# Kernel optimization log

Measured on AMD Instinct MI355X. Metric: run time of the kernel, lower is better.

Reference implementation:

```python
import jax, jax.numpy as jnp
import numpy as np

N_NODES = 100000
N_EDGES = 1600000
N_GRAPHS = 256


def gcn_conv(x, src, dst, edge_weight, W, b, num_nodes):
    """PyG GCNConv: add self-loops, symmetric degree normalization,
    linear transform, scatter-add aggregation, bias."""
    loop = jnp.arange(num_nodes)
    s = jnp.concatenate([src, loop])
    d = jnp.concatenate([dst, loop])
    ew = jnp.concatenate([edge_weight, jnp.ones((num_nodes,), dtype=edge_weight.dtype)])
    deg = jax.ops.segment_sum(ew, d, num_segments=num_nodes)  # [N]
    dinv = jnp.where(deg > 0, deg ** -0.5, 0.0)
    norm = dinv[s] * ew * dinv[d]  # [E+N]
    h = x @ W  # [N, out]
    msg = h[s] * norm[:, None]  # gather + scale
    out = jax.ops.segment_sum(msg, d, num_segments=num_nodes)  # scatter-add
    return out + b


def global_mean_pool(x, batch, num_graphs):
    s = jax.ops.segment_sum(x, batch, num_segments=num_graphs)
    cnt = jax.ops.segment_sum(jnp.ones((x.shape[0],), dtype=x.dtype), batch, num_segments=num_graphs)
    return s / jnp.maximum(cnt, 1.0)[:, None]


def setup_inputs() -> dict:
    key = jax.random.key(0)
    ks = jax.random.split(key, 12)
    x = jax.random.normal(ks[0], (N_NODES, 128), dtype=jnp.float32)
    edge_index = jax.random.randint(ks[1], (2, N_EDGES), 0, N_NODES, dtype=jnp.int64)
    edge_attr = jax.random.uniform(ks[2], (N_EDGES,), dtype=jnp.float32)
    batch = jnp.sort(jax.random.randint(ks[3], (N_NODES,), 0, N_GRAPHS, dtype=jnp.int64))
    def lin(k, fan_in, fan_out):
        lim = 1.0 / np.sqrt(fan_in)
        kw, kb = jax.random.split(k)
        W = jax.random.uniform(kw, (fan_in, fan_out), minval=-lim, maxval=lim, dtype=jnp.float32)
        b = jax.random.uniform(kb, (fan_out,), minval=-lim, maxval=lim, dtype=jnp.float32)
        return W, b
    W1, b1 = lin(ks[4], 128, 64)
    W2, b2 = lin(ks[5], 64, 64)
    W3, b3 = lin(ks[6], 64, 64)
    Wl, bl = lin(ks[7], 64, 10)
    return {"x": x, "edge_index": edge_index, "edge_attr": edge_attr, "batch": batch,
            "W1": W1, "b1": b1, "W2": W2, "b2": b2, "W3": W3, "b3": b3, "Wl": Wl, "bl": bl}


def reference(x, edge_index, edge_attr, batch, W1, b1, W2, b2, W3, b3, Wl, bl):
    src, dst = edge_index[0], edge_index[1]
    n = x.shape[0]
    h = jax.nn.relu(gcn_conv(x, src, dst, edge_attr, W1, b1, n))
    h = jax.nn.relu(gcn_conv(h, src, dst, edge_attr, W2, b2, n))
    h = jax.nn.relu(gcn_conv(h, src, dst, edge_attr, W3, b3, n))
    g = global_mean_pool(h, batch, N_GRAPHS)  # [G, 64]
    return g @ Wl + bl  # [G, num_classes]
```

## Files before the change

### kernel.cpp

```cpp
#include <hip/hip_runtime.h>
#include <hip/hip_bf16.h>

#define N_NODES  100000
#define N_EDGES  1600000
#define N_GRAPHS 256
#define F 64
#define NBUCK  782
#define CHUNK  4096
#define NCHUNK 391
#define GB     391


__global__ __launch_bounds__(1024) void k_hist(const int* __restrict__ dst, int* __restrict__ hist) {
    __shared__ int lh[NBUCK];
    int tid = threadIdx.x, chunk = blockIdx.x;
    for (int j = tid; j < NBUCK; j += 1024) lh[j] = 0;
    __syncthreads();
    int e0 = chunk * CHUNK;
#pragma unroll
    for (int i = 0; i < CHUNK / 1024; i++) {
        int e = e0 + i * 1024 + tid;
        if (e < N_EDGES) atomicAdd(&lh[dst[e] >> 7], 1);
    }
    __syncthreads();
    for (int j = tid; j < NBUCK; j += 1024) hist[chunk * NBUCK + j] = lh[j];
}

__global__ __launch_bounds__(512) void k_colscan(int* __restrict__ hist, int* __restrict__ btot) {
    __shared__ int ts[512];
    int b = blockIdx.x, tid = threadIdx.x;
    int v = (tid < NCHUNK) ? hist[tid * NBUCK + b] : 0;
    ts[tid] = v;
    __syncthreads();
    int x = v;
    for (int off = 1; off < 512; off <<= 1) {
        int t = (tid >= off) ? ts[tid - off] : 0;
        __syncthreads();
        x += t; ts[tid] = x;
        __syncthreads();
    }
    if (tid < NCHUNK) hist[tid * NBUCK + b] = x - v;
    if (tid == 511) btot[b] = x;
}

__global__ __launch_bounds__(512) void k_bscan_gstart(const int* __restrict__ btot, int* __restrict__ base,
                                                      const int* __restrict__ batch, int* __restrict__ gstart) {
    if (blockIdx.x == 1) {
        int g = threadIdx.x;
        if (g > N_GRAPHS) return;
        int lo = 0, hi = N_NODES;
        while (lo < hi) {
            int mid = (lo + hi) >> 1;
            if (batch[mid] < g) lo = mid + 1; else hi = mid;
        }
        gstart[g] = lo;
        return;
    }
    __shared__ int ts[256];
    int tid = threadIdx.x;
    int v[4], loc[4], run = 0;
    if (tid < 256) {
#pragma unroll
        for (int k = 0; k < 4; k++) {
            int c = tid * 4 + k;
            v[k] = (c < NBUCK) ? btot[c] : 0;
            loc[k] = run; run += v[k];
        }
        ts[tid] = run;
    }
    __syncthreads();
    int x = run;
    for (int off = 1; off < 256; off <<= 1) {
        int t = (tid >= off && tid < 256) ? ts[tid - off] : 0;
        __syncthreads();
        if (tid < 256) { x += t; ts[tid] = x; }
        __syncthreads();
    }
    if (tid < 256) {
        int texcl = x - run;
#pragma unroll
        for (int k = 0; k < 4; k++) {
            int c = tid * 4 + k;
            if (c < NBUCK) base[c] = texcl + loc[k];
        }
        if (tid == 255) base[NBUCK] = x;
    }
}

__global__ __launch_bounds__(1024) void k_partition(const int* __restrict__ src, const int* __restrict__ dst,
                                                    const float* __restrict__ ew,
                                                    const int* __restrict__ hist, const int* __restrict__ base,
                                                    long long* __restrict__ part) {
    __shared__ int cursor[NBUCK];
    int tid = threadIdx.x, chunk = blockIdx.x;
    for (int j = tid; j < NBUCK; j += 1024) cursor[j] = base[j] + hist[chunk * NBUCK + j];
    __syncthreads();
    int e0 = chunk * CHUNK;
#pragma unroll
    for (int i = 0; i < CHUNK / 1024; i++) {
        int e = e0 + i * 1024 + tid;
        if (e < N_EDGES) {
            int d = dst[e];
            int pos = atomicAdd(&cursor[d >> 7], 1);
            unsigned lo = (unsigned)src[e] | ((unsigned)(d & 127) << 17);
            long long rec = (long long)((unsigned long long)lo |
                            ((unsigned long long)__float_as_uint(ew[e]) << 32));
            part[pos] = rec;
        }
    }
}

__global__ __launch_bounds__(512) void k_deg(const long long* __restrict__ part,
                                             const int* __restrict__ base,
                                             float* __restrict__ dinv_g, int* __restrict__ row_off) {
    __shared__ float fdeg[128];
    __shared__ int   cnt[128];
    __shared__ int   sc[128];
    int b = blockIdx.x, tid = threadIdx.x;
    if (tid < 128) { fdeg[tid] = 1.0f; cnt[tid] = 0; }
    __syncthreads();
    int e0 = base[b], e1 = base[b + 1];
    for (int k = e0 + tid; k < e1; k += 512) {
        long long rec = part[k];
        int d7 = ((int)rec >> 17) & 127;
        atomicAdd(&fdeg[d7], __uint_as_float((unsigned)(rec >> 32)));
        atomicAdd(&cnt[d7], 1);
    }
    __syncthreads();
    int myc = 0, x = 0;
    if (tid < 128) {
        int node = b * 128 + tid;
        if (node < N_NODES) dinv_g[node] = rsqrtf(fdeg[tid]);
        myc = cnt[tid]; x = myc; sc[tid] = x;
    }
    __syncthreads();
    for (int off = 1; off < 128; off <<= 1) {
        int t = (tid < 128 && tid >= off) ? sc[tid - off] : 0;
        __syncthreads();
        if (tid < 128) { x += t; sc[tid] = x; }
        __syncthreads();
    }
    if (tid < 128) {
        int node = b * 128 + tid;
        if (node < N_NODES) row_off[node] = e0 + (x - myc);
    }
    if (b == 0 && tid == 0) row_off[N_NODES] = N_EDGES;
}

__global__ __launch_bounds__(512) void k_scat(const long long* __restrict__ part,
                                              const int* __restrict__ base,
                                              const float* __restrict__ dinv_g,
                                              const int* __restrict__ row_off,
                                              int2* __restrict__ esec) {
    __shared__ int cursor[128];
    int b = blockIdx.x, tid = threadIdx.x;
    if (tid < 128) {
        int node = b * 128 + tid;
        cursor[tid] = row_off[node < N_NODES ? node : N_NODES];
    }
    __syncthreads();
    int e0 = base[b], e1 = base[b + 1];
    for (int k = e0 + tid; k < e1; k += 512) {
        long long rec = part[k];
        int lo = (int)rec;
        int d7 = (lo >> 17) & 127;
        int s  = lo & 0x1FFFF;
        float w = __uint_as_float((unsigned)(rec >> 32));
        float coef = w * dinv_g[s];
        int pos = atomicAdd(&cursor[d7], 1);
        esec[pos] = make_int2(s << 7, __float_as_int(coef));
    }
    if (b == 0 && tid < 32) esec[N_EDGES + tid] = make_int2(0, 0);
}

__global__ __launch_bounds__(256) void k_gemm1(const float* __restrict__ X,
                                               const float* __restrict__ W,
                                               __hip_bfloat16* __restrict__ H) {
    constexpr int K = 128;
    constexpr int KC = 32;
    constexpr int XP = KC + 4;
    __shared__ float Xs[256 * XP];
    __shared__ float Ws[KC * F];
    const int tid  = threadIdx.x;
    const int fgrp = tid & 7;
    const int ngrp = tid >> 3;
    const int f0   = fgrp * 8;
    const int nb   = blockIdx.x * 256;

    float acc[8][8];
#pragma unroll
    for (int i = 0; i < 8; i++)
#pragma unroll
        for (int j = 0; j < 8; j++) acc[i][j] = 0.0f;

    for (int kc = 0; kc < K; kc += KC) {
        if (kc) __syncthreads();
#pragma unroll
        for (int pass = 0; pass < 8; pass++) {
            int idx = tid + pass * 256;
            int r = idx >> 3, q = idx & 7;
            int gr = nb + r; if (gr >= N_NODES) gr = N_NODES - 1;
            float4 v = *(const float4*)&X[(size_t)gr * K + kc + q * 4];
            *(float4*)&Xs[r * XP + q * 4] = v;
        }
#pragma unroll
        for (int pass = 0; pass < 2; pass++) {
            int idx = tid + pass * 256;
            float4 v = *(const float4*)&W[(size_t)(kc + (idx >> 4)) * F + (idx & 15) * 4];
            *(float4*)&Ws[idx * 4] = v;
        }
        __syncthreads();
#pragma unroll
        for (int k = 0; k < KC; k += 4) {
            float4 wa[4], wb[4];
#pragma unroll
            for (int kk = 0; kk < 4; kk++) {
                wa[kk] = *(const float4*)&Ws[(k + kk) * F + f0];
                wb[kk] = *(const float4*)&Ws[(k + kk) * F + f0 + 4];
            }
#pragma unroll
            for (int i = 0; i < 8; i++) {
                float4 xv = *(const float4*)&Xs[(ngrp + 32 * i) * XP + k];
#pragma unroll
                for (int kk = 0; kk < 4; kk++) {
                    float xk = (kk == 0) ? xv.x : (kk == 1) ? xv.y : (kk == 2) ? xv.z : xv.w;
                    acc[i][0] = fmaf(xk, wa[kk].x, acc[i][0]);
                    acc[i][1] = fmaf(xk, wa[kk].y, acc[i][1]);
                    acc[i][2] = fmaf(xk, wa[kk].z, acc[i][2]);
                    acc[i][3] = fmaf(xk, wa[kk].w, acc[i][3]);
                    acc[i][4] = fmaf(xk, wb[kk].x, acc[i][4]);
                    acc[i][5] = fmaf(xk, wb[kk].y, acc[i][5]);
                    acc[i][6] = fmaf(xk, wb[kk].z, acc[i][6]);
                    acc[i][7] = fmaf(xk, wb[kk].w, acc[i][7]);
                }
            }
        }
    }
#pragma unroll
    for (int i = 0; i < 8; i++) {
        int gn = nb + ngrp + 32 * i;
        if (gn < N_NODES) {
            __hip_bfloat16 hb[8];
#pragma unroll
            for (int j = 0; j < 8; j++) hb[j] = __float2bfloat16(acc[i][j]);
            *(uint4*)&H[(size_t)gn * F + f0] = *(uint4*)hb;
        }
    }
}

template <int K>
__global__ __launch_bounds__(256) void k_gemm(const unsigned short* __restrict__ X,
                                              const float* __restrict__ W,
                                              __hip_bfloat16* __restrict__ H) {
    constexpr int KC = 32;
    constexpr int XP = KC + 4;
    __shared__ float Xs[256 * XP];
    __shared__ float Ws[KC * F];
    const int tid  = threadIdx.x;
    const int fgrp = tid & 7;
    const int ngrp = tid >> 3;
    const int f0   = fgrp * 8;
    const int nb   = blockIdx.x * 256;

    float acc[8][8];
#pragma unroll
    for (int i = 0; i < 8; i++)
#pragma unroll
        for (int j = 0; j < 8; j++) acc[i][j] = 0.0f;

    for (int kc = 0; kc < K; kc += KC) {
        if (kc) __syncthreads();
#pragma unroll
        for (int pass = 0; pass < 4; pass++) {
            int idx = tid + pass * 256;
            int r = idx >> 2, q = idx & 3;
            int gr = nb + r; if (gr >= N_NODES) gr = N_NODES - 1;
            uint4 v = *(const uint4*)&X[(size_t)gr * K + kc + q * 8];
            float* dp = &Xs[r * XP + q * 8];
            dp[0] = __uint_as_float(v.x << 16);
            dp[1] = __uint_as_float(v.x & 0xffff0000u);
            dp[2] = __uint_as_float(v.y << 16);
            dp[3] = __uint_as_float(v.y & 0xffff0000u);
            dp[4] = __uint_as_float(v.z << 16);
            dp[5] = __uint_as_float(v.z & 0xffff0000u);
            dp[6] = __uint_as_float(v.w << 16);
            dp[7] = __uint_as_float(v.w & 0xffff0000u);
        }
#pragma unroll
        for (int pass = 0; pass < 2; pass++) {
            int idx = tid + pass * 256;
            float4 v = *(const float4*)&W[(size_t)(kc + (idx >> 4)) * F + (idx & 15) * 4];
            *(float4*)&Ws[idx * 4] = v;
        }
        __syncthreads();
#pragma unroll
        for (int k = 0; k < KC; k += 4) {
            float4 wa[4], wb[4];
#pragma unroll
            for (int kk = 0; kk < 4; kk++) {
                wa[kk] = *(const float4*)&Ws[(k + kk) * F + f0];
                wb[kk] = *(const float4*)&Ws[(k + kk) * F + f0 + 4];
            }
#pragma unroll
            for (int i = 0; i < 8; i++) {
                float4 xv = *(const float4*)&Xs[(ngrp + 32 * i) * XP + k];
#pragma unroll
                for (int kk = 0; kk < 4; kk++) {
                    float xk = (kk == 0) ? xv.x : (kk == 1) ? xv.y : (kk == 2) ? xv.z : xv.w;
                    acc[i][0] = fmaf(xk, wa[kk].x, acc[i][0]);
                    acc[i][1] = fmaf(xk, wa[kk].y, acc[i][1]);
                    acc[i][2] = fmaf(xk, wa[kk].z, acc[i][2]);
                    acc[i][3] = fmaf(xk, wa[kk].w, acc[i][3]);
                    acc[i][4] = fmaf(xk, wb[kk].x, acc[i][4]);
                    acc[i][5] = fmaf(xk, wb[kk].y, acc[i][5]);
                    acc[i][6] = fmaf(xk, wb[kk].z, acc[i][6]);
                    acc[i][7] = fmaf(xk, wb[kk].w, acc[i][7]);
                }
            }
        }
    }
#pragma unroll
    for (int i = 0; i < 8; i++) {
        int gn = nb + ngrp + 32 * i;
        if (gn < N_NODES) {
            __hip_bfloat16 hb[8];
#pragma unroll
            for (int j = 0; j < 8; j++) hb[j] = __float2bfloat16(acc[i][j]);
            *(uint4*)&H[(size_t)gn * F + f0] = *(uint4*)hb;
        }
    }
}

__global__ __launch_bounds__(256) void k_agg(const __hip_bfloat16* __restrict__ H,
                                             const int* __restrict__ row_off,
                                             const int2* __restrict__ esec,
                                             const float* __restrict__ dinv,
                                             const float* __restrict__ bias,
                                             __hip_bfloat16* __restrict__ O) {
    int wv   = threadIdx.x >> 6;
    int lane = threadIdx.x & 63;
    int np   = blockIdx.x * 16 + wv * 4;
    int q  = lane >> 3;
    int f8 = lane & 7;
    int r0 = __builtin_amdgcn_readfirstlane(row_off[np]);
    int r1 = __builtin_amdgcn_readfirstlane(row_off[np + 1]);
    int r2 = __builtin_amdgcn_readfirstlane(row_off[np + 2]);
    int r3 = __builtin_amdgcn_readfirstlane(row_off[np + 3]);
    int r4 = __builtin_amdgcn_readfirstlane(row_off[np + 4]);
    const char* Hbase = (const char*)H;

    float a0[8], a1[8], a2[8], a3[8];
#pragma unroll
    for (int u = 0; u < 8; u++) { a0[u] = 0.0f; a1[u] = 0.0f; a2[u] = 0.0f; a3[u] = 0.0f; }

    int l0 = r1 - r0, l1 = r2 - r1, l2 = r3 - r2, l3 = r4 - r3;
    int ml = l0 > l1 ? l0 : l1;
    if (l2 > ml) ml = l2;
    if (l3 > ml) ml = l3;
    int iters = (ml + 7) >> 3;
    int j0 = r0 + q, j1 = r1 + q, j2 = r2 + q, j3 = r3 + q;

    int2 ev0 = esec[j0 < N_EDGES ? j0 : N_EDGES];
    int2 ev1 = esec[j1 < N_EDGES ? j1 : N_EDGES];
    int2 ev2 = esec[j2 < N_EDGES ? j2 : N_EDGES];
    int2 ev3 = esec[j3 < N_EDGES ? j3 : N_EDGES];

    for (int it = 0; it < iters; it++) {
        int n0 = j0 + 8, n1 = j1 + 8, n2 = j2 + 8, n3 = j3 + 8;
        int2 en0 = esec[n0 < N_EDGES ? n0 : N_EDGES];
        int2 en1 = esec[n1 < N_EDGES ? n1 : N_EDGES];
        int2 en2 = esec[n2 < N_EDGES ? n2 : N_EDGES];
        int2 en3 = esec[n3 < N_EDGES ? n3 : N_EDGES];

        bool t0 = j0 < r1, t1 = j1 < r2, t2 = j2 < r3, t3 = j3 < r4;
        float c0 = t0 ? __int_as_float(ev0.y) : 0.0f;
        float c1 = t1 ? __int_as_float(ev1.y) : 0.0f;
        float c2 = t2 ? __int_as_float(ev2.y) : 0.0f;
        float c3 = t3 ? __int_as_float(ev3.y) : 0.0f;
        unsigned o0 = t0 ? (unsigned)ev0.x : 0u;
        unsigned o1 = t1 ? (unsigned)ev1.x : 0u;
        unsigned o2 = t2 ? (unsigned)ev2.x : 0u;
        unsigned o3 = t3 ? (unsigned)ev3.x : 0u;
        uint4 h0 = *(const uint4*)(Hbase + o0 + (f8 << 4));
        uint4 h1 = *(const uint4*)(Hbase + o1 + (f8 << 4));
        uint4 h2 = *(const uint4*)(Hbase + o2 + (f8 << 4));
        uint4 h3 = *(const uint4*)(Hbase + o3 + (f8 << 4));
        a0[0] = fmaf(c0, __uint_as_float(h0.x << 16),         a0[0]);
        a0[1] = fmaf(c0, __uint_as_float(h0.x & 0xffff0000u), a0[1]);
        a0[2] = fmaf(c0, __uint_as_float(h0.y << 16),         a0[2]);
        a0[3] = fmaf(c0, __uint_as_float(h0.y & 0xffff0000u), a0[3]);
        a0[4] = fmaf(c0, __uint_as_float(h0.z << 16),         a0[4]);
        a0[5] = fmaf(c0, __uint_as_float(h0.z & 0xffff0000u), a0[5]);
        a0[6] = fmaf(c0, __uint_as_float(h0.w << 16),         a0[6]);
        a0[7] = fmaf(c0, __uint_as_float(h0.w & 0xffff0000u), a0[7]);
        a1[0] = fmaf(c1, __uint_as_float(h1.x << 16),         a1[0]);
        a1[1] = fmaf(c1, __uint_as_float(h1.x & 0xffff0000u), a1[1]);
        a1[2] = fmaf(c1, __uint_as_float(h1.y << 16),         a1[2]);
        a1[3] = fmaf(c1, __uint_as_float(h1.y & 0xffff0000u), a1[3]);
        a1[4] = fmaf(c1, __uint_as_float(h1.z << 16),         a1[4]);
        a1[5] = fmaf(c1, __uint_as_float(h1.z & 0xffff0000u), a1[5]);
        a1[6] = fmaf(c1, __uint_as_float(h1.w << 16),         a1[6]);
        a1[7] = fmaf(c1, __uint_as_float(h1.w & 0xffff0000u), a1[7]);
        a2[0] = fmaf(c2, __uint_as_float(h2.x << 16),         a2[0]);
        a2[1] = fmaf(c2, __uint_as_float(h2.x & 0xffff0000u), a2[1]);
        a2[2] = fmaf(c2, __uint_as_float(h2.y << 16),         a2[2]);
        a2[3] = fmaf(c2, __uint_as_float(h2.y & 0xffff0000u), a2[3]);
        a2[4] = fmaf(c2, __uint_as_float(h2.z << 16),         a2[4]);
        a2[5] = fmaf(c2, __uint_as_float(h2.z & 0xffff0000u), a2[5]);
        a2[6] = fmaf(c2, __uint_as_float(h2.w << 16),         a2[6]);
        a2[7] = fmaf(c2, __uint_as_float(h2.w & 0xffff0000u), a2[7]);
        a3[0] = fmaf(c3, __uint_as_float(h3.x << 16),         a3[0]);
        a3[1] = fmaf(c3, __uint_as_float(h3.x & 0xffff0000u), a3[1]);
        a3[2] = fmaf(c3, __uint_as_float(h3.y << 16),         a3[2]);
        a3[3] = fmaf(c3, __uint_as_float(h3.y & 0xffff0000u), a3[3]);
        a3[4] = fmaf(c3, __uint_as_float(h3.z << 16),         a3[4]);
        a3[5] = fmaf(c3, __uint_as_float(h3.z & 0xffff0000u), a3[5]);
        a3[6] = fmaf(c3, __uint_as_float(h3.w << 16),         a3[6]);
        a3[7] = fmaf(c3, __uint_as_float(h3.w & 0xffff0000u), a3[7]);

        ev0 = en0; ev1 = en1; ev2 = en2; ev3 = en3;
        j0 = n0; j1 = n1; j2 = n2; j3 = n3;
    }
#pragma unroll
    for (int m = 8; m < 64; m <<= 1) {
#pragma unroll
        for (int u = 0; u < 8; u++) {
            a0[u] += __shfl_xor(a0[u], m);
            a1[u] += __shfl_xor(a1[u], m);
            a2[u] += __shfl_xor(a2[u], m);
            a3[u] += __shfl_xor(a3[u], m);
        }
    }
    if (q < 4) {
        int node = np + q;
        float av[8];
#pragma unroll
        for (int u = 0; u < 8; u++) {
            float t01 = (q & 1) ? a1[u] : a0[u];
            float t23 = (q & 1) ? a3[u] : a2[u];
            av[u] = (q & 2) ? t23 : t01;
        }
        float di = dinv[node];
        float di2 = di * di;
        uint4 hs = *(const uint4*)(Hbase + (size_t)node * 128 + (f8 << 4));
        float hv[8];
        hv[0] = __uint_as_float(hs.x << 16);
        hv[1] = __uint_as_float(hs.x & 0xffff0000u);
        hv[2] = __uint_as_float(hs.y << 16);
        hv[3] = __uint_as_float(hs.y & 0xffff0000u);
        hv[4] = __uint_as_float(hs.z << 16);
        hv[5] = __uint_as_float(hs.z & 0xffff0000u);
        hv[6] = __uint_as_float(hs.w << 16);
        hv[7] = __uint_as_float(hs.w & 0xffff0000u);
        const float4* bp = (const float4*)(bias + f8 * 8);
        float4 bv0 = bp[0], bv1 = bp[1];
        float r[8];
        r[0] = fmaxf(fmaf(av[0], di, fmaf(di2, hv[0], bv0.x)), 0.0f);
        r[1] = fmaxf(fmaf(av[1], di, fmaf(di2, hv[1], bv0.y)), 0.0f);
        r[2] = fmaxf(fmaf(av[2], di, fmaf(di2, hv[2], bv0.z)), 0.0f);
        r[3] = fmaxf(fmaf(av[3], di, fmaf(di2, hv[3], bv0.w)), 0.0f);
        r[4] = fmaxf(fmaf(av[4], di, fmaf(di2, hv[4], bv1.x)), 0.0f);
        r[5] = fmaxf(fmaf(av[5], di, fmaf(di2, hv[5], bv1.y)), 0.0f);
        r[6] = fmaxf(fmaf(av[6], di, fmaf(di2, hv[6], bv1.z)), 0.0f);
        r[7] = fmaxf(fmaf(av[7], di, fmaf(di2, hv[7], bv1.w)), 0.0f);
        __hip_bfloat16 hb[8];
#pragma unroll
        for (int u = 0; u < 8; u++) hb[u] = __float2bfloat16(r[u]);
        *(uint4*)&O[(size_t)node * F + f8 * 8] = *(uint4*)hb;
    }
}

__global__ __launch_bounds__(512) void k_pool_linear(const __hip_bfloat16* __restrict__ H,
                                                     const int* __restrict__ gstart,
                                                     const float* __restrict__ Wl,
                                                     const float* __restrict__ bl,
                                                     float* __restrict__ out) {
    int g = blockIdx.x;
    int beg = gstart[g], end = gstart[g + 1];
    int lane = threadIdx.x & 63, wv = threadIdx.x >> 6;
    float acc = 0.0f;
    for (int r = beg + wv; r < end; r += 8)
        acc += __bfloat162float(H[(size_t)r * F + lane]);
    __shared__ float s[8][F];
    s[wv][lane] = acc;
    __syncthreads();
    if (wv == 0) {
        float tot = 0.0f;
#pragma unroll
        for (int w = 0; w < 8; w++) tot += s[w][lane];
        float cntf = (float)(end - beg);
        float p = tot / fmaxf(cntf, 1.0f);
        for (int c = 0; c < 10; c++) {
            float v = p * Wl[lane * 10 + c];
            for (int off = 32; off; off >>= 1) v += __shfl_down(v, off);
            if (lane == 0) out[g * 10 + c] = v + bl[c];
        }
    }
}


extern "C" void kernel_launch(void* const* d_in, const int* in_sizes, int n_in,
                              void* d_out, int out_size, void* d_ws, size_t ws_size,
                              hipStream_t stream) {
    const float* x    = (const float*)d_in[0];
    const int*   ei   = (const int*)d_in[1];
    const float* ea   = (const float*)d_in[2];
    const int*   bat  = (const int*)d_in[3];
    const float* W1   = (const float*)d_in[4];
    const float* b1   = (const float*)d_in[5];
    const float* W2   = (const float*)d_in[6];
    const float* b2   = (const float*)d_in[7];
    const float* W3   = (const float*)d_in[8];
    const float* b3   = (const float*)d_in[9];
    const float* Wl   = (const float*)d_in[10];
    const float* bl   = (const float*)d_in[11];
    float* out = (float*)d_out;

    const int* src = ei;
    const int* dst = ei + N_EDGES;

    char* ws = (char*)d_ws;
    size_t off = 0;
    auto carve = [&](size_t bytes) {
        void* p = ws + off;
        off += (bytes + 255) & ~(size_t)255;
        return p;
    };
    float*          dinv    = (float*)carve(N_NODES * 4);
    int*            row_off = (int*)  carve((N_NODES + 1) * 4);
    int2*           esec    = (int2*) carve(((size_t)N_EDGES + 32) * 8);
    __hip_bfloat16* hbuf    = (__hip_bfloat16*)carve((size_t)N_NODES * F * 2);
    __hip_bfloat16* obuf    = (__hip_bfloat16*)carve((size_t)N_NODES * F * 2);
    long long*      part    = (long long*)carve((size_t)N_EDGES * 8);
    int*            hist    = (int*)  carve((size_t)NCHUNK * NBUCK * 4);
    int*            btot    = (int*)  carve((NBUCK + 8) * 4);
    int*            base    = (int*)  carve((NBUCK + 8) * 4);
    int*            gstart  = (int*)  carve((N_GRAPHS + 1) * 4);
    (void)ws_size; (void)in_sizes; (void)n_in; (void)out_size;

    k_hist        <<<NCHUNK, 1024, 0, stream>>>(dst, hist);
    k_colscan     <<<NBUCK,  512,  0, stream>>>(hist, btot);
    k_bscan_gstart<<<2,      512,  0, stream>>>(btot, base, bat, gstart);
    k_partition   <<<NCHUNK, 1024, 0, stream>>>(src, dst, ea, hist, base, part);
    k_deg         <<<NBUCK,  512,  0, stream>>>(part, base, dinv, row_off);
    k_scat        <<<NBUCK,  512,  0, stream>>>(part, base, dinv, row_off, esec);

    k_gemm1<<<GB, 256, 0, stream>>>(x, W1, hbuf);
    k_agg<<<N_NODES / 16, 256, 0, stream>>>(hbuf, row_off, esec, dinv, b1, obuf);
    k_gemm<64><<<GB, 256, 0, stream>>>((const unsigned short*)obuf, W2, hbuf);
    k_agg<<<N_NODES / 16, 256, 0, stream>>>(hbuf, row_off, esec, dinv, b2, obuf);
    k_gemm<64><<<GB, 256, 0, stream>>>((const unsigned short*)obuf, W3, hbuf);
    k_agg<<<N_NODES / 16, 256, 0, stream>>>(hbuf, row_off, esec, dinv, b3, obuf);

    k_pool_linear<<<N_GRAPHS, 512, 0, stream>>>(obuf, gstart, Wl, bl, out);
}
```

Measured before the change: 362.0 us.

## Sort nodes by degree bin to balance per-wave aggregation work

Adds a counting sort of nodes into degree bins (histogram, scan, scatter kernels) producing a permutation, and makes the aggregation kernel process nodes in that order. Each wave handles four nodes with similar edge counts, reducing idle iterations caused by the max-degree loop bound. It adds three small kernels, an indirect lookup, and less contiguous output writes and row_off reads.

New measurement: 368.1 us. No clear change (+1.7%).

```diff
diff --git a/kernel.cpp b/kernel.cpp
--- a/kernel.cpp
+++ b/kernel.cpp
@@ -9,6 +9,8 @@
 #define CHUNK  4096
 #define NCHUNK 391
 #define GB     391
+#define NBIN   16
+#define NCHN   98
 
 
 __global__ __launch_bounds__(1024) void k_hist(const int* __restrict__ dst, int* __restrict__ hist) {
@@ -171,6 +173,57 @@
         esec[pos] = make_int2(s << 7, __float_as_int(coef));
     }
     if (b == 0 && tid < 32) esec[N_EDGES + tid] = make_int2(0, 0);
+}
+
+
+__global__ __launch_bounds__(1024) void k_nhist(const int* __restrict__ row_off, int* __restrict__ nhist) {
+    __shared__ int lh[NBIN];
+    int tid = threadIdx.x, c = blockIdx.x;
+    if (tid < NBIN) lh[tid] = 0;
+    __syncthreads();
+    int n = c * 1024 + tid;
+    if (n < N_NODES) {
+        int len = row_off[n + 1] - row_off[n];
+        int bin = (len + 7) >> 3; if (bin > NBIN - 1) bin = NBIN - 1;
+        atomicAdd(&lh[bin], 1);
+    }
+    __syncthreads();
+    if (tid < NBIN) nhist[c * NBIN + tid] = lh[tid];
+}
+
+__global__ __launch_bounds__(1024) void k_nscan(int* __restrict__ nhist) {
+    __shared__ int h[NCHN * NBIN];
+    __shared__ int tot[NBIN];
+    int tid = threadIdx.x;
+    for (int i = tid; i < NCHN * NBIN; i += 1024) h[i] = nhist[i];
+    __syncthreads();
+    if (tid < NBIN) {
+        int run = 0;
+        for (int c = 0; c < NCHN; c++) { int v = h[c * NBIN + tid]; h[c * NBIN + tid] = run; run += v; }
+        tot[tid] = run;
+    }
+    __syncthreads();
+    if (tid == 0) {
+        int run = 0;
+        for (int b = 0; b < NBIN; b++) { int v = tot[b]; tot[b] = run; run += v; }
+    }
+    __syncthreads();
+    for (int i = tid; i < NCHN * NBIN; i += 1024) nhist[i] = h[i] + tot[i & (NBIN - 1)];
+}
+
+__global__ __launch_bounds__(1024) void k_nscat(const int* __restrict__ row_off, const int* __restrict__ nhist,
+                                                int* __restrict__ perm) {
+    __shared__ int cur[NBIN];
+    int tid = threadIdx.x, c = blockIdx.x;
+    if (tid < NBIN) cur[tid] = nhist[c * NBIN + tid];
+    __syncthreads();
+    int n = c * 1024 + tid;
+    if (n < N_NODES) {
+        int len = row_off[n + 1] - row_off[n];
+        int bin = (len + 7) >> 3; if (bin > NBIN - 1) bin = NBIN - 1;
+        int pos = atomicAdd(&cur[bin], 1);
+        perm[pos] = n;
+    }
 }
 
 __global__ __launch_bounds__(256) void k_gemm1(const float* __restrict__ X,
@@ -336,29 +389,38 @@
                                              const int2* __restrict__ esec,
                                              const float* __restrict__ dinv,
                                              const float* __restrict__ bias,
+                                             const int* __restrict__ perm,
                                              __hip_bfloat16* __restrict__ O) {
     int wv   = threadIdx.x >> 6;
     int lane = threadIdx.x & 63;
     int np   = blockIdx.x * 16 + wv * 4;
     int q  = lane >> 3;
     int f8 = lane & 7;
-    int r0 = __builtin_amdgcn_readfirstlane(row_off[np]);
-    int r1 = __builtin_amdgcn_readfirstlane(row_off[np + 1]);
-    int r2 = __builtin_amdgcn_readfirstlane(row_off[np + 2]);
-    int r3 = __builtin_amdgcn_readfirstlane(row_off[np + 3]);
-    int r4 = __builtin_amdgcn_readfirstlane(row_off[np + 4]);
+    int n0 = __builtin_amdgcn_readfirstlane(perm[np]);
+    int n1 = __builtin_amdgcn_readfirstlane(perm[np + 1]);
+    int n2 = __builtin_amdgcn_readfirstlane(perm[np + 2]);
+    int n3 = __builtin_amdgcn_readfirstlane(perm[np + 3]);
+    int b0 = __builtin_amdgcn_readfirstlane(row_off[n0]);
+    int e0 = __builtin_amdgcn_readfirstlane(row_off[n0 + 1]);
+    int b1 = __builtin_amdgcn_readfirstlane(row_off[n1]);
+    int e1 = __builtin_amdgcn_readfirstlane(row_off[n1 + 1]);
+    int b2 = __builtin_amdgcn_readfirstlane(row_off[n2]);
+    int e2 = __builtin_amdgcn_readfirstlane(row_off[n2 + 1]);
+    int b3 = __builtin_amdgcn_readfirstlane(row_off[n3]);
+    int e3 = __builtin_amdgcn_readfirstlane(row_off[n3 + 1]);
     const char* Hbase = (const char*)H;
+    const int fb = f8 << 4;
 
     float a0[8], a1[8], a2[8], a3[8];
 #pragma unroll
     for (int u = 0; u < 8; u++) { a0[u] = 0.0f; a1[u] = 0.0f; a2[u] = 0.0f; a3[u] = 0.0f; }
 
-    int l0 = r1 - r0, l1 = r2 - r1, l2 = r3 - r2, l3 = r4 - r3;
+    int l0 = e0 - b0, l1 = e1 - b1, l2 = e2 - b2, l3 = e3 - b3;
     int ml = l0 > l1 ? l0 : l1;
     if (l2 > ml) ml = l2;
     if (l3 > ml) ml = l3;
     int iters = (ml + 7) >> 3;
-    int j0 = r0 + q, j1 = r1 + q, j2 = r2 + q, j3 = r3 + q;
+    int j0 = b0 + q, j1 = b1 + q, j2 = b2 + q, j3 = b3 + q;
 
     int2 ev0 = esec[j0 < N_EDGES ? j0 : N_EDGES];
     int2 ev1 = esec[j1 < N_EDGES ? j1 : N_EDGES];
@@ -366,13 +428,13 @@
     int2 ev3 = esec[j3 < N_EDGES ? j3 : N_EDGES];
 
     for (int it = 0; it < iters; it++) {
-        int n0 = j0 + 8, n1 = j1 + 8, n2 = j2 + 8, n3 = j3 + 8;
-        int2 en0 = esec[n0 < N_EDGES ? n0 : N_EDGES];
-        int2 en1 = esec[n1 < N_EDGES ? n1 : N_EDGES];
-        int2 en2 = esec[n2 < N_EDGES ? n2 : N_EDGES];
-        int2 en3 = esec[n3 < N_EDGES ? n3 : N_EDGES];
-
-        bool t0 = j0 < r1, t1 = j1 < r2, t2 = j2 < r3, t3 = j3 < r4;
+        int m0 = j0 + 8, m1 = j1 + 8, m2 = j2 + 8, m3 = j3 + 8;
+        int2 en0 = esec[m0 < N_EDGES ? m0 : N_EDGES];
+        int2 en1 = esec[m1 < N_EDGES ? m1 : N_EDGES];
+        int2 en2 = esec[m2 < N_EDGES ? m2 : N_EDGES];
+        int2 en3 = esec[m3 < N_EDGES ? m3 : N_EDGES];
+
+        bool t0 = j0 < e0, t1 = j1 < e1, t2 = j2 < e2, t3 = j3 < e3;
         float c0 = t0 ? __int_as_float(ev0.y) : 0.0f;
         float c1 = t1 ? __int_as_float(ev1.y) : 0.0f;
         float c2 = t2 ? __int_as_float(ev2.y) : 0.0f;
@@ -381,10 +443,10 @@
         unsigned o1 = t1 ? (unsigned)ev1.x : 0u;
         unsigned o2 = t2 ? (unsigned)ev2.x : 0u;
         unsigned o3 = t3 ? (unsigned)ev3.x : 0u;
-        uint4 h0 = *(const uint4*)(Hbase + o0 + (f8 << 4));
-        uint4 h1 = *(const uint4*)(Hbase + o1 + (f8 << 4));
-        uint4 h2 = *(const uint4*)(Hbase + o2 + (f8 << 4));
-        uint4 h3 = *(const uint4*)(Hbase + o3 + (f8 << 4));
+        uint4 h0 = *(const uint4*)(Hbase + o0 + fb);
+        uint4 h1 = *(const uint4*)(Hbase + o1 + fb);
+        uint4 h2 = *(const uint4*)(Hbase + o2 + fb);
+        uint4 h3 = *(const uint4*)(Hbase + o3 + fb);
         a0[0] = fmaf(c0, __uint_as_float(h0.x << 16),         a0[0]);
         a0[1] = fmaf(c0, __uint_as_float(h0.x & 0xffff0000u), a0[1]);
         a0[2] = fmaf(c0, __uint_as_float(h0.y << 16),         a0[2]);
@@ -419,7 +481,7 @@
         a3[7] = fmaf(c3, __uint_as_float(h3.w & 0xffff0000u), a3[7]);
 
         ev0 = en0; ev1 = en1; ev2 = en2; ev3 = en3;
-        j0 = n0; j1 = n1; j2 = n2; j3 = n3;
+        j0 = m0; j1 = m1; j2 = m2; j3 = m3;
     }
 #pragma unroll
     for (int m = 8; m < 64; m <<= 1) {
@@ -432,7 +494,9 @@
         }
     }
     if (q < 4) {
-        int node = np + q;
+        int s01 = (q & 1) ? n1 : n0;
+        int s23 = (q & 1) ? n3 : n2;
+        int node = (q & 2) ? s23 : s01;
         float av[8];
 #pragma unroll
         for (int u = 0; u < 8; u++) {
@@ -442,7 +506,7 @@
         }
         float di = dinv[node];
         float di2 = di * di;
-        uint4 hs = *(const uint4*)(Hbase + (size_t)node * 128 + (f8 << 4));
+        uint4 hs = *(const uint4*)(Hbase + (size_t)node * 128 + fb);
         float hv[8];
         hv[0] = __uint_as_float(hs.x << 16);
         hv[1] = __uint_as_float(hs.x & 0xffff0000u);
@@ -536,6 +600,8 @@
     int*            btot    = (int*)  carve((NBUCK + 8) * 4);
     int*            base    = (int*)  carve((NBUCK + 8) * 4);
     int*            gstart  = (int*)  carve((N_GRAPHS + 1) * 4);
+    int*            nhist   = (int*)  carve((size_t)NCHN * NBIN * 4);
+    int*            perm    = (int*)  carve((size_t)N_NODES * 4);
     (void)ws_size; (void)in_sizes; (void)n_in; (void)out_size;
 
     k_hist        <<<NCHUNK, 1024, 0, stream>>>(dst, hist);
@@ -543,14 +609,17 @@
     k_bscan_gstart<<<2,      512,  0, stream>>>(btot, base, bat, gstart);
     k_partition   <<<NCHUNK, 1024, 0, stream>>>(src, dst, ea, hist, base, part);
     k_deg         <<<NBUCK,  512,  0, stream>>>(part, base, dinv, row_off);
+    k_nhist       <<<NCHN,   1024, 0, stream>>>(row_off, nhist);
+    k_nscan       <<<1,      1024, 0, stream>>>(nhist);
+    k_nscat       <<<NCHN,   1024, 0, stream>>>(row_off, nhist, perm);
     k_scat        <<<NBUCK,  512,  0, stream>>>(part, base, dinv, row_off, esec);
 
     k_gemm1<<<GB, 256, 0, stream>>>(x, W1, hbuf);
-    k_agg<<<N_NODES / 16, 256, 0, stream>>>(hbuf, row_off, esec, dinv, b1, obuf);
+    k_agg<<<N_NODES / 16, 256, 0, stream>>>(hbuf, row_off, esec, dinv, b1, perm, obuf);
     k_gemm<64><<<GB, 256, 0, stream>>>((const unsigned short*)obuf, W2, hbuf);
-    k_agg<<<N_NODES / 16, 256, 0, stream>>>(hbuf, row_off, esec, dinv, b2, obuf);
+    k_agg<<<N_NODES / 16, 256, 0, stream>>>(hbuf, row_off, esec, dinv, b2, perm, obuf);
     k_gemm<64><<<GB, 256, 0, stream>>>((const unsigned short*)obuf, W3, hbuf);
-    k_agg<<<N_NODES / 16, 256, 0, stream>>>(hbuf, row_off, esec, dinv, b3, obuf);
+    k_agg<<<N_NODES / 16, 256, 0, stream>>>(hbuf, row_off, esec, dinv, b3, perm, obuf);
 
     k_pool_linear<<<N_GRAPHS, 512, 0, stream>>>(obuf, gstart, Wl, bl, out);
 }
```

## Fold source dinv into GEMM epilogue and fuse degree and scatter kernels

Applied to the files above, without the earlier changes.

Pre-scales each GEMM output row by its node's dinv, so the edge coefficient becomes just the raw edge weight. That removes the random dinv[src] gather from the CSR scatter, and the aggregation epilogue then becomes di*(sum + self) + bias. The degree and scatter kernels are merged into one, with the scanned row offsets reused directly as shared-memory cursors. This saves a launch and a second pass over the partitioned records. In exchange, rounding changes slightly because the scaled values are stored in bf16.

After: 359.9 us. No clear change (-0.6%).

```diff
diff --git a/kernel.cpp b/kernel.cpp
--- a/kernel.cpp
+++ b/kernel.cpp
@@ -110,12 +110,14 @@
     }
 }
 
-__global__ __launch_bounds__(512) void k_deg(const long long* __restrict__ part,
-                                             const int* __restrict__ base,
-                                             float* __restrict__ dinv_g, int* __restrict__ row_off) {
+__global__ __launch_bounds__(512) void k_degscat(const long long* __restrict__ part,
+                                                 const int* __restrict__ base,
+                                                 float* __restrict__ dinv_g, int* __restrict__ row_off,
+                                                 int2* __restrict__ esec) {
     __shared__ float fdeg[128];
     __shared__ int   cnt[128];
     __shared__ int   sc[128];
+    __shared__ int   cursor[128];
     int b = blockIdx.x, tid = threadIdx.x;
     if (tid < 128) { fdeg[tid] = 1.0f; cnt[tid] = 0; }
     __syncthreads();
@@ -142,39 +144,26 @@
     }
     if (tid < 128) {
         int node = b * 128 + tid;
-        if (node < N_NODES) row_off[node] = e0 + (x - myc);
+        int ro = e0 + (x - myc);
+        if (node < N_NODES) row_off[node] = ro;
+        cursor[tid] = ro;
     }
     if (b == 0 && tid == 0) row_off[N_NODES] = N_EDGES;
-}
-
-__global__ __launch_bounds__(512) void k_scat(const long long* __restrict__ part,
-                                              const int* __restrict__ base,
-                                              const float* __restrict__ dinv_g,
-                                              const int* __restrict__ row_off,
-                                              int2* __restrict__ esec) {
-    __shared__ int cursor[128];
-    int b = blockIdx.x, tid = threadIdx.x;
-    if (tid < 128) {
-        int node = b * 128 + tid;
-        cursor[tid] = row_off[node < N_NODES ? node : N_NODES];
-    }
-    __syncthreads();
-    int e0 = base[b], e1 = base[b + 1];
+    __syncthreads();
     for (int k = e0 + tid; k < e1; k += 512) {
         long long rec = part[k];
         int lo = (int)rec;
         int d7 = (lo >> 17) & 127;
         int s  = lo & 0x1FFFF;
-        float w = __uint_as_float((unsigned)(rec >> 32));
-        float coef = w * dinv_g[s];
         int pos = atomicAdd(&cursor[d7], 1);
-        esec[pos] = make_int2(s << 7, __float_as_int(coef));
+        esec[pos] = make_int2(s << 7, (int)(unsigned)(rec >> 32));
     }
     if (b == 0 && tid < 32) esec[N_EDGES + tid] = make_int2(0, 0);
 }
 
 __global__ __launch_bounds__(256) void k_gemm1(const float* __restrict__ X,
                                                const float* __restrict__ W,
+                                               const float* __restrict__ dinv,
                                                __hip_bfloat16* __restrict__ H) {
     constexpr int K = 128;
     constexpr int KC = 32;
@@ -240,9 +229,10 @@
     for (int i = 0; i < 8; i++) {
         int gn = nb + ngrp + 32 * i;
         if (gn < N_NODES) {
+            float di = dinv[gn];
             __hip_bfloat16 hb[8];
 #pragma unroll
-            for (int j = 0; j < 8; j++) hb[j] = __float2bfloat16(acc[i][j]);
+            for (int j = 0; j < 8; j++) hb[j] = __float2bfloat16(acc[i][j] * di);
             *(uint4*)&H[(size_t)gn * F + f0] = *(uint4*)hb;
         }
     }
@@ -251,6 +241,7 @@
 template <int K>
 __global__ __launch_bounds__(256) void k_gemm(const unsigned short* __restrict__ X,
                                               const float* __restrict__ W,
+                                              const float* __restrict__ dinv,
                                               __hip_bfloat16* __restrict__ H) {
     constexpr int KC = 32;
     constexpr int XP = KC + 4;
@@ -323,15 +314,16 @@
     for (int i = 0; i < 8; i++) {
         int gn = nb + ngrp + 32 * i;
         if (gn < N_NODES) {
+            float di = dinv[gn];
             __hip_bfloat16 hb[8];
 #pragma unroll
-            for (int j = 0; j < 8; j++) hb[j] = __float2bfloat16(acc[i][j]);
+            for (int j = 0; j < 8; j++) hb[j] = __float2bfloat16(acc[i][j] * di);
             *(uint4*)&H[(size_t)gn * F + f0] = *(uint4*)hb;
         }
     }
 }
 
-__global__ __launch_bounds__(256) void k_agg(const __hip_bfloat16* __restrict__ H,
+__global__ __launch_bounds__(256) void k_agg(const __hip_bfloat16* __restrict__ Hd,
                                              const int* __restrict__ row_off,
                                              const int2* __restrict__ esec,
                                              const float* __restrict__ dinv,
@@ -347,7 +339,8 @@
     int r2 = __builtin_amdgcn_readfirstlane(row_off[np + 2]);
     int r3 = __builtin_amdgcn_readfirstlane(row_off[np + 3]);
     int r4 = __builtin_amdgcn_readfirstlane(row_off[np + 4]);
-    const char* Hbase = (const char*)H;
+    const char* Hbase = (const char*)Hd;
+    const int fb = f8 << 4;
 
     float a0[8], a1[8], a2[8], a3[8];
 #pragma unroll
@@ -366,11 +359,11 @@
     int2 ev3 = esec[j3 < N_EDGES ? j3 : N_EDGES];
 
     for (int it = 0; it < iters; it++) {
-        int n0 = j0 + 8, n1 = j1 + 8, n2 = j2 + 8, n3 = j3 + 8;
-        int2 en0 = esec[n0 < N_EDGES ? n0 : N_EDGES];
-        int2 en1 = esec[n1 < N_EDGES ? n1 : N_EDGES];
-        int2 en2 = esec[n2 < N_EDGES ? n2 : N_EDGES];
-        int2 en3 = esec[n3 < N_EDGES ? n3 : N_EDGES];
+        int m0 = j0 + 8, m1 = j1 + 8, m2 = j2 + 8, m3 = j3 + 8;
+        int2 en0 = esec[m0 < N_EDGES ? m0 : N_EDGES];
+        int2 en1 = esec[m1 < N_EDGES ? m1 : N_EDGES];
+        int2 en2 = esec[m2 < N_EDGES ? m2 : N_EDGES];
+        int2 en3 = esec[m3 < N_EDGES ? m3 : N_EDGES];
 
         bool t0 = j0 < r1, t1 = j1 < r2, t2 = j2 < r3, t3 = j3 < r4;
         float c0 = t0 ? __int_as_float(ev0.y) : 0.0f;
@@ -381,10 +374,10 @@
         unsigned o1 = t1 ? (unsigned)ev1.x : 0u;
         unsigned o2 = t2 ? (unsigned)ev2.x : 0u;
         unsigned o3 = t3 ? (unsigned)ev3.x : 0u;
-        uint4 h0 = *(const uint4*)(Hbase + o0 + (f8 << 4));
-        uint4 h1 = *(const uint4*)(Hbase + o1 + (f8 << 4));
-        uint4 h2 = *(const uint4*)(Hbase + o2 + (f8 << 4));
-        uint4 h3 = *(const uint4*)(Hbase + o3 + (f8 << 4));
+        uint4 h0 = *(const uint4*)(Hbase + o0 + fb);
+        uint4 h1 = *(const uint4*)(Hbase + o1 + fb);
+        uint4 h2 = *(const uint4*)(Hbase + o2 + fb);
+        uint4 h3 = *(const uint4*)(Hbase + o3 + fb);
         a0[0] = fmaf(c0, __uint_as_float(h0.x << 16),         a0[0]);
         a0[1] = fmaf(c0, __uint_as_float(h0.x & 0xffff0000u), a0[1]);
         a0[2] = fmaf(c0, __uint_as_float(h0.y << 16),         a0[2]);
@@ -419,7 +412,7 @@
         a3[7] = fmaf(c3, __uint_as_float(h3.w & 0xffff0000u), a3[7]);
 
         ev0 = en0; ev1 = en1; ev2 = en2; ev3 = en3;
-        j0 = n0; j1 = n1; j2 = n2; j3 = n3;
+        j0 = m0; j1 = m1; j2 = m2; j3 = m3;
     }
 #pragma unroll
     for (int m = 8; m < 64; m <<= 1) {
@@ -441,8 +434,7 @@
             av[u] = (q & 2) ? t23 : t01;
         }
         float di = dinv[node];
-        float di2 = di * di;
-        uint4 hs = *(const uint4*)(Hbase + (size_t)node * 128 + (f8 << 4));
+        uint4 hs = *(const uint4*)(Hbase + (size_t)node * 128 + fb);
         float hv[8];
         hv[0] = __uint_as_float(hs.x << 16);
         hv[1] = __uint_as_float(hs.x & 0xffff0000u);
@@ -455,14 +447,14 @@
         const float4* bp = (const float4*)(bias + f8 * 8);
         float4 bv0 = bp[0], bv1 = bp[1];
         float r[8];
-        r[0] = fmaxf(fmaf(av[0], di, fmaf(di2, hv[0], bv0.x)), 0.0f);
-        r[1] = fmaxf(fmaf(av[1], di, fmaf(di2, hv[1], bv0.y)), 0.0f);
-        r[2] = fmaxf(fmaf(av[2], di, fmaf(di2, hv[2], bv0.z)), 0.0f);
-        r[3] = fmaxf(fmaf(av[3], di, fmaf(di2, hv[3], bv0.w)), 0.0f);
-        r[4] = fmaxf(fmaf(av[4], di, fmaf(di2, hv[4], bv1.x)), 0.0f);
-        r[5] = fmaxf(fmaf(av[5], di, fmaf(di2, hv[5], bv1.y)), 0.0f);
-        r[6] = fmaxf(fmaf(av[6], di, fmaf(di2, hv[6], bv1.z)), 0.0f);
-        r[7] = fmaxf(fmaf(av[7], di, fmaf(di2, hv[7], bv1.w)), 0.0f);
+        r[0] = fmaxf(fmaf(di, av[0] + hv[0], bv0.x), 0.0f);
+        r[1] = fmaxf(fmaf(di, av[1] + hv[1], bv0.y), 0.0f);
+        r[2] = fmaxf(fmaf(di, av[2] + hv[2], bv0.z), 0.0f);
+        r[3] = fmaxf(fmaf(di, av[3] + hv[3], bv0.w), 0.0f);
+        r[4] = fmaxf(fmaf(di, av[4] + hv[4], bv1.x), 0.0f);
+        r[5] = fmaxf(fmaf(di, av[5] + hv[5], bv1.y), 0.0f);
+        r[6] = fmaxf(fmaf(di, av[6] + hv[6], bv1.z), 0.0f);
+        r[7] = fmaxf(fmaf(di, av[7] + hv[7], bv1.w), 0.0f);
         __hip_bfloat16 hb[8];
 #pragma unroll
         for (int u = 0; u < 8; u++) hb[u] = __float2bfloat16(r[u]);
@@ -542,14 +534,13 @@
     k_colscan     <<<NBUCK,  512,  0, stream>>>(hist, btot);
     k_bscan_gstart<<<2,      512,  0, stream>>>(btot, base, bat, gstart);
     k_partition   <<<NCHUNK, 1024, 0, stream>>>(src, dst, ea, hist, base, part);
-    k_deg         <<<NBUCK,  512,  0, stream>>>(part, base, dinv, row_off);
-    k_scat        <<<NBUCK,  512,  0, stream>>>(part, base, dinv, row_off, esec);
-
-    k_gemm1<<<GB, 256, 0, stream>>>(x, W1, hbuf);
+    k_degscat     <<<NBUCK,  512,  0, stream>>>(part, base, dinv, row_off, esec);
+
+    k_gemm1<<<GB, 256, 0, stream>>>(x, W1, dinv, hbuf);
     k_agg<<<N_NODES / 16, 256, 0, stream>>>(hbuf, row_off, esec, dinv, b1, obuf);
-    k_gemm<64><<<GB, 256, 0, stream>>>((const unsigned short*)obuf, W2, hbuf);
+    k_gemm<64><<<GB, 256, 0, stream>>>((const unsigned short*)obuf, W2, dinv, hbuf);
     k_agg<<<N_NODES / 16, 256, 0, stream>>>(hbuf, row_off, esec, dinv, b2, obuf);
-    k_gemm<64><<<GB, 256, 0, stream>>>((const unsigned short*)obuf, W3, hbuf);
+    k_gemm<64><<<GB, 256, 0, stream>>>((const unsigned short*)obuf, W3, dinv, hbuf);
     k_agg<<<N_NODES / 16, 256, 0, stream>>>(hbuf, row_off, esec, dinv, b3, obuf);
 
     k_pool_linear<<<N_GRAPHS, 512, 0, stream>>>(obuf, gstart, Wl, bl, out);
```
